# Performance work log

Measured on AMD Instinct MI355X. Metric: run time of the kernel, lower is better.

## Reference

```python
import jax, jax.numpy as jnp
import numpy as np

DIM = 384
NH = 16
HD = DIM // NH          # 24
HID = DIM * 4           # titan/cms hidden
RD = 2 * (HD // 3 // 2) # 8 rope channels per axis (d/h/w), 3*RD == HD


def _ln(x, scale, bias):
    m = x.mean(-1, keepdims=True)
    v = ((x - m) ** 2).mean(-1, keepdims=True)
    return (x - m) * jax.lax.rsqrt(v + 1e-5) * scale + bias


def _mlp(x, w1, b1, w2, b2):
    # TitanMemory / CMS level: Linear -> GELU -> Linear (titan_layers=2)
    h = jax.nn.gelu(x @ w1 + b1, approximate=False)
    return h @ w2 + b2


def _rotate(x, pos):
    # rotate_queries_or_keys: interleaved rotary. x: [B,nh,N,d], pos: [N]
    d = x.shape[-1]
    inv_freq = 1.0 / (10000.0 ** (jnp.arange(0, d, 2, dtype=jnp.float32) / d))
    ang = pos[:, None] * inv_freq[None, :]              # [N, d/2]
    sin, cos = jnp.sin(ang), jnp.cos(ang)
    x1, x2 = x[..., 0::2], x[..., 1::2]
    y1 = x1 * cos - x2 * sin
    y2 = x1 * sin + x2 * cos
    return jnp.stack([y1, y2], axis=-1).reshape(x.shape)


def _rope3d(q, T, H, W):
    # 3D RoPE on frame tokens (action_tokens=0): time / height / width axes
    B, N, D = q.shape
    qh = q.reshape(B, N, NH, HD).transpose(0, 2, 1, 3)   # [B,nh,N,hd]
    ids = jnp.arange(T * H * W)
    tpos = (ids // (H * W)).astype(jnp.float32)
    hpos = ((ids % (H * W)) // W).astype(jnp.float32)
    wpos = (ids % W).astype(jnp.float32)
    qd = _rotate(qh[..., :RD], tpos)
    qhh = _rotate(qh[..., RD:2 * RD], hpos)
    qww = _rotate(qh[..., 2 * RD:3 * RD], wpos)
    out = jnp.concatenate([qd, qhh, qww], axis=-1)
    return out.transpose(0, 2, 1, 3).reshape(B, N, D)


def setup_inputs() -> dict:
    key = jax.random.key(0)
    ks = jax.random.split(key, 8)
    B, T, H, W = 8, 8, 16, 16
    N = T * H * W
    p = lambda k, sh: jax.random.normal(k, sh, jnp.float32) * 0.02
    return {
        "x": jax.random.normal(ks[0], (B, N, DIM), jnp.float32),
        "norm1_scale": jnp.ones((DIM,), jnp.float32),
        "norm1_bias": jnp.zeros((DIM,), jnp.float32),
        "norm2_scale": jnp.ones((DIM,), jnp.float32),
        "norm2_bias": jnp.zeros((DIM,), jnp.float32),
        "q_w": p(ks[1], (DIM, DIM)),
        # stacked Titan memories: [M_k, M_v, M_eta, M_alpha, M_memory]
        "titan_w1": p(ks[2], (5, DIM, HID)),
        "titan_b1": jnp.zeros((5, HID), jnp.float32),
        "titan_w2": p(ks[3], (5, HID, DIM)),
        "titan_b2": jnp.zeros((5, DIM), jnp.float32),
        "out_w": p(ks[4], (DIM, DIM)),
        "out_b": jnp.zeros((DIM,), jnp.float32),
        # CMS levels: [fast, medium, slow]
        "cms_w1": p(ks[5], (3, DIM, HID)),
        "cms_b1": jnp.zeros((3, HID), jnp.float32),
        "cms_w2": p(ks[6], (3, HID, DIM)),
        "cms_b2": jnp.zeros((3, DIM), jnp.float32),
        "T": T, "H": H, "W": W, "action_tokens": 0,
    }


def reference(x, norm1_scale, norm1_bias, norm2_scale, norm2_bias, q_w,
              titan_w1, titan_b1, titan_w2, titan_b2, out_w, out_b,
              cms_w1, cms_b1, cms_w2, cms_b2, T, H, W, action_tokens):
    # Phase A: self-modifying Titan (eval path: retrieval only)
    y = _ln(x, norm1_scale, norm1_bias)
    q = y @ q_w                                  # static query projection (Eq. 76)
    q = _rope3d(q, T, H, W)                      # 3D RoPE (action_tokens == 0)
    out = _mlp(q, titan_w1[4], titan_b1[4], titan_w2[4], titan_b2[4])  # M_memory(q)
    out = out @ out_w + out_b                    # out_proj
    x = x + out                                  # residual (drop_path = identity)
    # Phase B: CMS multi-frequency MLP cascade
    y = _ln(x, norm2_scale, norm2_bias)
    cms = sum(_mlp(y, cms_w1[i], cms_b1[i], cms_w2[i], cms_b2[i]) for i in range(3))
    return x + cms
```

## Files before the change

### kernel.cpp

```cpp
#include <hip/hip_runtime.h>
#include <math.h>

typedef unsigned short u16;
typedef unsigned int u32;
typedef __attribute__((ext_vector_type(8))) short short8;
typedef __attribute__((ext_vector_type(4))) float f32x4;

#define DIM 384
#define HID 1536

static __device__ __forceinline__ float bf2f(u32 b){ return __uint_as_float(b << 16); }
static __device__ __forceinline__ u16 f2bf(float f){
  u32 u = __float_as_uint(f);
  u32 r = (u + 0x7fffu + ((u >> 16) & 1u)) >> 16;
  return (u16)r;
}
static __device__ __forceinline__ float gelu_fast(float v){
  float u = v * fmaf(0.0713548162726f, v * v, 1.59576912161f);
  float e = __builtin_amdgcn_exp2f(-1.44269504089f * u);
  return v * __builtin_amdgcn_rcpf(1.0f + e);
}
static __device__ __forceinline__ void gload_lds16(const u16* g, u16* l){
  __builtin_amdgcn_global_load_lds(
      (__attribute__((address_space(1))) void*)(void*)const_cast<u16*>(g),
      (__attribute__((address_space(3))) void*)(void*)l, 16, 0, 0);
}
template<int N> static __device__ __forceinline__ void vm_wait(){
  if constexpr (N == 0)      asm volatile("s_waitcnt vmcnt(0)" ::: "memory");
  else if constexpr (N == 5) asm volatile("s_waitcnt vmcnt(5)" ::: "memory");
  else if constexpr (N == 6) asm volatile("s_waitcnt vmcnt(6)" ::: "memory");
  else                       asm volatile("s_waitcnt vmcnt(0)" ::: "memory");
}
static __device__ __forceinline__ void barrier_raw(){
  asm volatile("s_barrier" ::: "memory");
}
static __device__ __forceinline__ void lgkm_wait0(){
  asm volatile("s_waitcnt lgkmcnt(0)" ::: "memory");
}

__global__ __launch_bounds__(256) void ln_kernel(const float* __restrict__ x,
    const float* __restrict__ sc, const float* __restrict__ bi, u16* __restrict__ y){
  int lane = threadIdx.x & 63;
  int row = blockIdx.x * 4 + (threadIdx.x >> 6);
  const float* xr = x + (size_t)row * DIM;
  float v[6];
  float s = 0.f, sq = 0.f;
#pragma unroll
  for (int i = 0; i < 6; ++i){
    float f = xr[lane + 64*i];
    v[i] = f; s += f; sq += f*f;
  }
#pragma unroll
  for (int o = 1; o < 64; o <<= 1){ s += __shfl_xor(s, o); sq += __shfl_xor(sq, o); }
  float mean = s * (1.0f/DIM);
  float var = sq * (1.0f/DIM) - mean*mean;
  float inv = rsqrtf(var + 1e-5f);
  u16* yr = y + (size_t)row * DIM;
#pragma unroll
  for (int i = 0; i < 6; ++i){
    int c = lane + 64*i;
    yr[c] = f2bf((v[i] - mean) * inv * sc[c] + bi[c]);
  }
}

__global__ __launch_bounds__(256) void rope_kernel(u16* __restrict__ q,
    const int* __restrict__ Tp, const int* __restrict__ Hp, const int* __restrict__ Wp,
    int Mtok){
  int idx = blockIdx.x * 256 + threadIdx.x;
  int tok = idx / 192;
  if (tok >= Mtok) return;
  int p = idx - tok * 192;
  int H = *Hp, W = *Wp, T = *Tp;
  int HW = H * W;
  int Ns = T * HW;
  int n = tok % Ns;
  int head = p / 12;
  int pp = p - head * 12;
  int s = pp >> 2, f = pp & 3;
  float pos;
  if (s == 0)      pos = (float)(n / HW);
  else if (s == 1) pos = (float)((n / W) % H);
  else             pos = (float)(n % W);
  const float LOG2_10000 = 13.28771237954945f;
  float inv = __builtin_amdgcn_exp2f(-0.25f * (float)f * LOG2_10000);
  float ang = pos * inv;
  float sn = __sinf(ang), cs = __cosf(ang);
  size_t base = (size_t)tok * DIM + head * 24 + s * 8 + 2 * f;
  u32 u = *(u32*)(q + base);
  float x1 = bf2f(u & 0xffffu), x2 = bf2f(u >> 16);
  float y1 = x1 * cs - x2 * sn;
  float y2 = x1 * sn + x2 * cs;
  *(u32*)(q + base) = (u32)f2bf(y1) | ((u32)f2bf(y2) << 16);
}

template<int R, int C>
__global__ __launch_bounds__(256) void transpose_kernel(
    const float* __restrict__ s0, const float* __restrict__ s1,
    const float* __restrict__ s2, const float* __restrict__ s3,
    u16* __restrict__ d0, u16* __restrict__ d1, u16* __restrict__ d2, u16* __restrict__ d3,
    int dstStride){
  const float* src = (blockIdx.z == 0) ? s0 : (blockIdx.z == 1) ? s1 : (blockIdx.z == 2) ? s2 : s3;
  u16* dst         = (blockIdx.z == 0) ? d0 : (blockIdx.z == 1) ? d1 : (blockIdx.z == 2) ? d2 : d3;
  __shared__ u16 t[32][33];
  int tx = threadIdx.x & 31, ty = threadIdx.x >> 5;
  int r0 = blockIdx.y * 32, c0 = blockIdx.x * 32;
#pragma unroll
  for (int i = 0; i < 4; ++i)
    t[ty + 8*i][tx] = f2bf(src[(size_t)(r0 + ty + 8*i) * C + c0 + tx]);
  __syncthreads();
#pragma unroll
  for (int i = 0; i < 4; ++i)
    dst[(size_t)(c0 + ty + 8*i) * dstStride + r0 + tx] = t[tx][ty + 8*i];
}

__global__ void bias3_kernel(const float* __restrict__ b, float* __restrict__ o){
  int n = threadIdx.x;
  o[n] = b[n] + b[384 + n] + b[768 + n];
}

enum { E_NONE = 0, E_BIAS = 1, E_RES_F32 = 3, E_FINAL = 5 };

template<int BM, int N, int K, int EPI>
__global__ __launch_bounds__(256) void gemm_kernel(
    const u16* __restrict__ A, const u16* __restrict__ Bt,
    void* __restrict__ Cv, const float* __restrict__ bias,
    const float* __restrict__ res, float* __restrict__ accbuf){
  constexpr int BN = 128, BK = 64;
  constexpr int MT = BM / 32, NT = 4;
  constexpr int AIT = BM / 32, BIT = 4;
  __shared__ __align__(16) u16 As[BM * BK];
  __shared__ __align__(16) u16 Bs[BN * BK];
  const int tid = threadIdx.x;
  const int lane = tid & 63;
  const int wv = tid >> 6;
  const int wm = (wv >> 1) * (BM / 2);
  const int wn = (wv & 1) * 64;
  const int quad = lane >> 4;
  const int l16 = lane & 15;
  const int rsw = l16 & 7;
  const size_t m0 = (size_t)blockIdx.x * BM;
  const int n0 = blockIdx.y * BN;
  const int srow = lane >> 3;
  const int scol = ((lane & 7) ^ srow) * 8;

  f32x4 acc[MT][NT];
  const f32x4 zero = {0.f, 0.f, 0.f, 0.f};
#pragma unroll
  for (int mt = 0; mt < MT; ++mt)
#pragma unroll
    for (int nt = 0; nt < NT; ++nt) acc[mt][nt] = zero;

  for (int kt = 0; kt < K; kt += BK){
#pragma unroll
    for (int i = 0; i < AIT; ++i){
      int seg = i * 4 + wv;
      gload_lds16(A + (m0 + (size_t)(seg * 8 + srow)) * K + kt + scol, As + seg * 512);
    }
#pragma unroll
    for (int i = 0; i < BIT; ++i){
      int seg = i * 4 + wv;
      gload_lds16(Bt + (size_t)(n0 + seg * 8 + srow) * K + kt + scol, Bs + seg * 512);
    }
    __syncthreads();
#pragma unroll
    for (int kk = 0; kk < 2; ++kk){
      short8 af[MT], bfr[NT];
#pragma unroll
      for (int mt = 0; mt < MT; ++mt)
        af[mt] = *(const short8*)(As + (wm + mt*16 + l16) * BK + (((kk*4 + quad) ^ rsw) << 3));
#pragma unroll
      for (int nt = 0; nt < NT; ++nt)
        bfr[nt] = *(const short8*)(Bs + (wn + nt*16 + l16) * BK + (((kk*4 + quad) ^ rsw) << 3));
#pragma unroll
      for (int mt = 0; mt < MT; ++mt)
#pragma unroll
        for (int nt = 0; nt < NT; ++nt)
          acc[mt][nt] = __builtin_amdgcn_mfma_f32_16x16x32_bf16(af[mt], bfr[nt], acc[mt][nt], 0, 0, 0);
    }
    __syncthreads();
  }

#pragma unroll
  for (int mt = 0; mt < MT; ++mt){
#pragma unroll
    for (int nt = 0; nt < NT; ++nt){
      int ncol = n0 + wn + nt*16 + l16;
      float bv = (EPI != E_NONE) ? bias[ncol] : 0.f;
      size_t mbase = m0 + wm + mt*16 + quad*4;
#pragma unroll
      for (int r = 0; r < 4; ++r){
        size_t off = (mbase + r) * N + ncol;
        float vv = acc[mt][nt][r];
        if      (EPI == E_NONE)      ((u16*)Cv)[off] = f2bf(vv);
        else if (EPI == E_BIAS)      ((u16*)Cv)[off] = f2bf(vv + bv);
        else          accbuf[off] = vv + bv + res[off];
      }
    }
  }
}

template<int HIDT, int NCH, int EPI>
__global__ __launch_bounds__(512, 2) void fused_mlp3_kernel(
    const u16* __restrict__ A, const u16* __restrict__ W1t, const u16* __restrict__ W2t,
    const float* __restrict__ b1, const float* __restrict__ b2,
    const float* __restrict__ accbuf, void* __restrict__ outp){
  __shared__ __align__(16) u16 ring[2][384 * 64];
  __shared__ __align__(16) u16 Hs[4 * 64 * 64];

  const int tid  = threadIdx.x;
  const int lane = tid & 63;
  const int wv   = tid >> 6;
  const int quad = lane >> 4;
  const int l16  = lane & 15;
  const int rsw  = l16 & 7;
  const size_t m0 = (size_t)blockIdx.x * 64;
  const int srow = lane >> 3;
  const int scol = ((lane & 7) ^ srow) * 8;
  const int uwm = (wv & 1) * 32;
  const int pan = wv >> 1;
  const int dwn = wv * 48;

  auto stage_up = [&](int hc, int kt, u16* buf){
#pragma unroll
    for (int i = 0; i < 5; ++i){
      int seg = i * 8 + wv;
      const u16* src = (i == 0)
          ? A + (m0 + (size_t)(wv * 8 + srow)) * 384 + kt * 64 + scol
          : W1t + ((size_t)hc + (seg - 8) * 8 + srow) * 384 + kt * 64 + scol;
      gload_lds16(src, buf + seg * 512);
    }
  };
  auto stage_dn = [&](int hc, int q, u16* buf){
#pragma unroll
    for (int i = 0; i < 6; ++i){
      int seg = i * 8 + wv;
      gload_lds16(W2t + (size_t)(seg * 8 + srow) * HIDT + hc + q * 64 + scol,
                  buf + seg * 512);
    }
  };

  f32x4 cacc[4][3];
  const f32x4 zero = {0.f, 0.f, 0.f, 0.f};
#pragma unroll
  for (int mt = 0; mt < 4; ++mt)
#pragma unroll
    for (int nt = 0; nt < 3; ++nt) cacc[mt][nt] = zero;

  stage_up(0, 0, ring[0]);

  for (int c = 0; c < NCH; ++c){
    const int hc = c * 256;
    f32x4 hacc[2][4];
#pragma unroll
    for (int mt = 0; mt < 2; ++mt)
#pragma unroll
      for (int nt = 0; nt < 4; ++nt) hacc[mt][nt] = zero;

#pragma unroll
    for (int kt = 0; kt < 6; ++kt){
      if (kt < 5){ stage_up(hc, kt + 1, ring[(kt + 1) & 1]); vm_wait<5>(); }
      else       { stage_dn(hc, 0, ring[0]);                 vm_wait<6>(); }
      barrier_raw();
      const u16* buf = ring[kt & 1];
#pragma unroll
      for (int kk = 0; kk < 2; ++kk){
        short8 af[2], bfr[4];
#pragma unroll
        for (int mt = 0; mt < 2; ++mt)
          af[mt] = *(const short8*)(buf + (uwm + mt*16 + l16) * 64 + (((kk*4 + quad) ^ rsw) << 3));
#pragma unroll
        for (int nt = 0; nt < 4; ++nt)
          bfr[nt] = *(const short8*)(buf + (64 + pan*64 + nt*16 + l16) * 64 + (((kk*4 + quad) ^ rsw) << 3));
#pragma unroll
        for (int mt = 0; mt < 2; ++mt)
#pragma unroll
          for (int nt = 0; nt < 4; ++nt)
            hacc[mt][nt] = __builtin_amdgcn_mfma_f32_16x16x32_bf16(af[mt], bfr[nt], hacc[mt][nt], 0, 0, 0);
      }
      barrier_raw();
    }

#pragma unroll
    for (int nt = 0; nt < 4; ++nt){
      int pc = nt*16 + l16;
      float bv = b1[hc + pan*64 + pc];
      u16* hp = Hs + pan*4096;
#pragma unroll
      for (int mt = 0; mt < 2; ++mt){
#pragma unroll
        for (int r = 0; r < 4; ++r){
          int row = uwm + mt*16 + quad*4 + r;
          hp[row*64 + (((pc >> 3) ^ (row & 7)) << 3) + (pc & 7)] = f2bf(gelu_fast(hacc[mt][nt][r] + bv));
        }
      }
    }
    lgkm_wait0();
    barrier_raw();

#pragma unroll
    for (int dt = 0; dt < 4; ++dt){
      if (dt < 3)            { stage_dn(hc, dt + 1, ring[(dt + 1) & 1]); vm_wait<6>(); }
      else if (c + 1 < NCH)  { stage_up(hc + 256, 0, ring[0]);           vm_wait<5>(); }
      else                   { vm_wait<0>(); }
      barrier_raw();
      const u16* buf = ring[dt & 1];
#pragma unroll
      for (int kk = 0; kk < 2; ++kk){
        short8 af[4], bfr[3];
#pragma unroll
        for (int mt = 0; mt < 4; ++mt)
          af[mt] = *(const short8*)(Hs + dt*4096 + (mt*16 + l16) * 64 + (((kk*4 + quad) ^ rsw) << 3));
#pragma unroll
        for (int nt = 0; nt < 3; ++nt)
          bfr[nt] = *(const short8*)(buf + (dwn + nt*16 + l16) * 64 + (((kk*4 + quad) ^ rsw) << 3));
#pragma unroll
        for (int mt = 0; mt < 4; ++mt)
#pragma unroll
          for (int nt = 0; nt < 3; ++nt)
            cacc[mt][nt] = __builtin_amdgcn_mfma_f32_16x16x32_bf16(af[mt], bfr[nt], cacc[mt][nt], 0, 0, 0);
      }
      barrier_raw();
    }
  }

#pragma unroll
  for (int nt = 0; nt < 3; ++nt){
    int col = dwn + nt*16 + l16;
    float bv = b2[col];
#pragma unroll
    for (int mt = 0; mt < 4; ++mt){
      size_t mbase = m0 + mt*16 + quad*4;
#pragma unroll
      for (int r = 0; r < 4; ++r){
        size_t off = (mbase + r) * DIM + col;
        float vv = cacc[mt][nt][r] + bv;
        if (EPI == E_BIAS) ((u16*)outp)[off] = f2bf(vv);
        else  ((float*)outp)[off] = accbuf[off] + vv;
      }
    }
  }
}

extern "C" void kernel_launch(void* const* d_in, const int* in_sizes, int n_in,
                              void* d_out, int out_size, void* d_ws, size_t ws_size,
                              hipStream_t stream) {
  const int W11 = DIM * HID;
  const float* x   = (const float*)d_in[0];
  const float* n1s = (const float*)d_in[1];
  const float* n1b = (const float*)d_in[2];
  const float* n2s = (const float*)d_in[3];
  const float* n2b = (const float*)d_in[4];
  const float* qw  = (const float*)d_in[5];
  const float* tw1 = (const float*)d_in[6] + 4 * W11;
  const float* tb1 = (const float*)d_in[7] + 4 * HID;
  const float* tw2 = (const float*)d_in[8] + 4 * W11;
  const float* tb2 = (const float*)d_in[9] + 4 * DIM;
  const float* ow  = (const float*)d_in[10];
  const float* ob  = (const float*)d_in[11];
  const float* cw1 = (const float*)d_in[12];
  const float* cb1 = (const float*)d_in[13];
  const float* cw2 = (const float*)d_in[14];
  const float* cb2 = (const float*)d_in[15];
  const int* Tp = (const int*)d_in[16];
  const int* Hp = (const int*)d_in[17];
  const int* Wp = (const int*)d_in[18];
  const int M = in_sizes[0] / DIM;

  char* ws = (char*)d_ws;
  if (ws_size < 22611456u) return;
  u16*  y    = (u16*) (ws + 0);
  u16*  qwT  = (u16*) (ws + 12582912);
  u16*  owT  = (u16*) (ws + 12877824);
  u16*  w1T  = (u16*) (ws + 13172736);
  u16*  w2T  = (u16*) (ws + 14352384);
  u16*  cw1T = (u16*) (ws + 15532032);
  u16*  cw2T = (u16*) (ws + 19070976);
  float* cb2s = (float*)(ws + 22609920);
  u16*  qb   = (u16*)d_out;

  transpose_kernel<384,384><<<dim3(12,12,2),256,0,stream>>>(
      qw, ow, qw, qw, qwT, owT, qwT, qwT, 384);
  transpose_kernel<384,1536><<<dim3(48,12,4),256,0,stream>>>(
      tw1, cw1, cw1 + W11, cw1 + 2*W11, w1T, cw1T, cw1T + W11, cw1T + 2*W11, 384);
  transpose_kernel<1536,384><<<dim3(12,48,1),256,0,stream>>>(
      tw2, tw2, tw2, tw2, w2T, w2T, w2T, w2T, 1536);
  transpose_kernel<1536,384><<<dim3(12,48,3),256,0,stream>>>(
      cw2, cw2 + W11, cw2 + 2*W11, cw2, cw2T, cw2T + 1536, cw2T + 3072, cw2T, 4608);
  bias3_kernel<<<1,384,0,stream>>>(cb2, cb2s);

  ln_kernel<<<M/4,256,0,stream>>>(x, n1s, n1b, y);
  gemm_kernel<64,384,384,E_NONE><<<dim3(M/64,3),256,0,stream>>>(y, qwT, qb, nullptr, nullptr, nullptr);
  rope_kernel<<<(M*192)/256,256,0,stream>>>(qb, Tp, Hp, Wp, M);
  fused_mlp3_kernel<1536,6,E_BIAS><<<M/64,512,0,stream>>>(
      qb, w1T, w2T, tb1, tb2, nullptr, y);
  gemm_kernel<64,384,384,E_RES_F32><<<dim3(M/64,3),256,0,stream>>>(
      y, owT, nullptr, ob, x, (float*)d_out);
  ln_kernel<<<M/4,256,0,stream>>>((const float*)d_out, n2s, n2b, y);
  fused_mlp3_kernel<4608,18,E_FINAL><<<M/64,512,0,stream>>>(
      y, cw1T, cw2T, cb1, cb2s, (const float*)d_out, d_out);
}
```

Measured before the change: 436.9 us.

## Keep A tile resident in LDS and stream W2 directly into registers

The fused MLP kernel now loads the 64x384 activation tile into shared memory once per block instead of re-staging it for every hidden chunk. The ring buffer holds only W1 tiles, and the next chunk's first W1 tile is prefetched during the last up-projection step. The down-projection no longer stages W2 through LDS with barriers; each wave loads its W2 fragments straight from global memory into double-buffered registers. This removes repeated A traffic and the barriers in the down phase, at the cost of uncoalesced, latency-exposed global loads of W2 and more LDS per block (As 48KB + ring 64KB + Hs 32KB), which may reduce occupancy.

```diff
diff --git a/kernel.cpp b/kernel.cpp
--- a/kernel.cpp
+++ b/kernel.cpp
@@ -27,6 +27,7 @@
 }
 template<int N> static __device__ __forceinline__ void vm_wait(){
   if constexpr (N == 0)      asm volatile("s_waitcnt vmcnt(0)" ::: "memory");
+  else if constexpr (N == 4) asm volatile("s_waitcnt vmcnt(4)" ::: "memory");
   else if constexpr (N == 5) asm volatile("s_waitcnt vmcnt(5)" ::: "memory");
   else if constexpr (N == 6) asm volatile("s_waitcnt vmcnt(6)" ::: "memory");
   else                       asm volatile("s_waitcnt vmcnt(0)" ::: "memory");
@@ -200,11 +201,12 @@
 }
 
 template<int HIDT, int NCH, int EPI>
-__global__ __launch_bounds__(512, 2) void fused_mlp3_kernel(
+__global__ __launch_bounds__(512, 2) void fused_mlp4_kernel(
     const u16* __restrict__ A, const u16* __restrict__ W1t, const u16* __restrict__ W2t,
     const float* __restrict__ b1, const float* __restrict__ b2,
     const float* __restrict__ accbuf, void* __restrict__ outp){
-  __shared__ __align__(16) u16 ring[2][384 * 64];
+  __shared__ __align__(16) u16 As[6 * 64 * 64];
+  __shared__ __align__(16) u16 ring[2][256 * 64];
   __shared__ __align__(16) u16 Hs[4 * 64 * 64];
 
   const int tid  = threadIdx.x;
@@ -222,22 +224,18 @@
 
   auto stage_up = [&](int hc, int kt, u16* buf){
 #pragma unroll
-    for (int i = 0; i < 5; ++i){
-      int seg = i * 8 + wv;
-      const u16* src = (i == 0)
-          ? A + (m0 + (size_t)(wv * 8 + srow)) * 384 + kt * 64 + scol
-          : W1t + ((size_t)hc + (seg - 8) * 8 + srow) * 384 + kt * 64 + scol;
-      gload_lds16(src, buf + seg * 512);
+    for (int i = 0; i < 4; ++i){
+      int rg = i * 8 + wv;
+      gload_lds16(W1t + ((size_t)hc + rg * 8 + srow) * 384 + kt * 64 + scol,
+                  buf + rg * 512);
     }
   };
-  auto stage_dn = [&](int hc, int q, u16* buf){
-#pragma unroll
-    for (int i = 0; i < 6; ++i){
-      int seg = i * 8 + wv;
-      gload_lds16(W2t + (size_t)(seg * 8 + srow) * HIDT + hc + q * 64 + scol,
-                  buf + seg * 512);
-    }
-  };
+
+#pragma unroll
+  for (int i = 0; i < 6; ++i)
+    gload_lds16(A + (m0 + (size_t)(wv * 8 + srow)) * 384 + i * 64 + scol,
+                As + (i * 8 + wv) * 512);
+  stage_up(0, 0, ring[0]);
 
   f32x4 cacc[4][3];
   const f32x4 zero = {0.f, 0.f, 0.f, 0.f};
@@ -245,8 +243,6 @@
   for (int mt = 0; mt < 4; ++mt)
 #pragma unroll
     for (int nt = 0; nt < 3; ++nt) cacc[mt][nt] = zero;
-
-  stage_up(0, 0, ring[0]);
 
   for (int c = 0; c < NCH; ++c){
     const int hc = c * 256;
@@ -258,8 +254,9 @@
 
 #pragma unroll
     for (int kt = 0; kt < 6; ++kt){
-      if (kt < 5){ stage_up(hc, kt + 1, ring[(kt + 1) & 1]); vm_wait<5>(); }
-      else       { stage_dn(hc, 0, ring[0]);                 vm_wait<6>(); }
+      if (kt < 5)           { stage_up(hc, kt + 1, ring[(kt + 1) & 1]); vm_wait<4>(); }
+      else if (c + 1 < NCH) { stage_up(hc + 256, 0, ring[0]);           vm_wait<4>(); }
+      else                  { vm_wait<0>(); }
       barrier_raw();
       const u16* buf = ring[kt & 1];
 #pragma unroll
@@ -267,10 +264,10 @@
         short8 af[2], bfr[4];
 #pragma unroll
         for (int mt = 0; mt < 2; ++mt)
-          af[mt] = *(const short8*)(buf + (uwm + mt*16 + l16) * 64 + (((kk*4 + quad) ^ rsw) << 3));
+          af[mt] = *(const short8*)(As + kt*4096 + (uwm + mt*16 + l16) * 64 + (((kk*4 + quad) ^ rsw) << 3));
 #pragma unroll
         for (int nt = 0; nt < 4; ++nt)
-          bfr[nt] = *(const short8*)(buf + (64 + pan*64 + nt*16 + l16) * 64 + (((kk*4 + quad) ^ rsw) << 3));
+          bfr[nt] = *(const short8*)(buf + (pan*64 + nt*16 + l16) * 64 + (((kk*4 + quad) ^ rsw) << 3));
 #pragma unroll
         for (int mt = 0; mt < 2; ++mt)
 #pragma unroll
@@ -297,29 +294,28 @@
     lgkm_wait0();
     barrier_raw();
 
-#pragma unroll
-    for (int dt = 0; dt < 4; ++dt){
-      if (dt < 3)            { stage_dn(hc, dt + 1, ring[(dt + 1) & 1]); vm_wait<6>(); }
-      else if (c + 1 < NCH)  { stage_up(hc + 256, 0, ring[0]);           vm_wait<5>(); }
-      else                   { vm_wait<0>(); }
-      barrier_raw();
-      const u16* buf = ring[dt & 1];
-#pragma unroll
-      for (int kk = 0; kk < 2; ++kk){
-        short8 af[4], bfr[3];
-#pragma unroll
-        for (int mt = 0; mt < 4; ++mt)
-          af[mt] = *(const short8*)(Hs + dt*4096 + (mt*16 + l16) * 64 + (((kk*4 + quad) ^ rsw) << 3));
+    short8 wb[2][3];
+#pragma unroll
+    for (int nt = 0; nt < 3; ++nt)
+      wb[0][nt] = *(const short8*)(W2t + (size_t)(dwn + nt*16 + l16) * HIDT + hc + quad*8);
+#pragma unroll
+    for (int s = 0; s < 8; ++s){
+      if (s < 7){
+        int off = ((s+1) >> 1) * 64 + (((s+1) & 1) * 4 + quad) * 8;
 #pragma unroll
         for (int nt = 0; nt < 3; ++nt)
-          bfr[nt] = *(const short8*)(buf + (dwn + nt*16 + l16) * 64 + (((kk*4 + quad) ^ rsw) << 3));
-#pragma unroll
-        for (int mt = 0; mt < 4; ++mt)
-#pragma unroll
-          for (int nt = 0; nt < 3; ++nt)
-            cacc[mt][nt] = __builtin_amdgcn_mfma_f32_16x16x32_bf16(af[mt], bfr[nt], cacc[mt][nt], 0, 0, 0);
-      }
-      barrier_raw();
+          wb[(s+1) & 1][nt] = *(const short8*)(W2t + (size_t)(dwn + nt*16 + l16) * HIDT + hc + off);
+      }
+      int dt = s >> 1, kk = s & 1;
+      short8 af[4];
+#pragma unroll
+      for (int mt = 0; mt < 4; ++mt)
+        af[mt] = *(const short8*)(Hs + dt*4096 + (mt*16 + l16) * 64 + (((kk*4 + quad) ^ rsw) << 3));
+#pragma unroll
+      for (int mt = 0; mt < 4; ++mt)
+#pragma unroll
+        for (int nt = 0; nt < 3; ++nt)
+          cacc[mt][nt] = __builtin_amdgcn_mfma_f32_16x16x32_bf16(af[mt], wb[s & 1][nt], cacc[mt][nt], 0, 0, 0);
     }
   }
 
@@ -391,11 +387,11 @@
   ln_kernel<<<M/4,256,0,stream>>>(x, n1s, n1b, y);
   gemm_kernel<64,384,384,E_NONE><<<dim3(M/64,3),256,0,stream>>>(y, qwT, qb, nullptr, nullptr, nullptr);
   rope_kernel<<<(M*192)/256,256,0,stream>>>(qb, Tp, Hp, Wp, M);
-  fused_mlp3_kernel<1536,6,E_BIAS><<<M/64,512,0,stream>>>(
+  fused_mlp4_kernel<1536,6,E_BIAS><<<M/64,512,0,stream>>>(
       qb, w1T, w2T, tb1, tb2, nullptr, y);
   gemm_kernel<64,384,384,E_RES_F32><<<dim3(M/64,3),256,0,stream>>>(
       y, owT, nullptr, ob, x, (float*)d_out);
   ln_kernel<<<M/4,256,0,stream>>>((const float*)d_out, n2s, n2b, y);
-  fused_mlp3_kernel<4608,18,E_FINAL><<<M/64,512,0,stream>>>(
+  fused_mlp4_kernel<4608,18,E_FINAL><<<M/64,512,0,stream>>>(
       y, cw1T, cw2T, cb1, cb2s, (const float*)d_out, d_out);
 }
```

After: 450.8 us. 1.03x slower.
